# Performance work log

Measured on AMD Instinct MI355X. Metric: run time of the kernel, lower is better.

## Reference

```python
import jax, jax.numpy as jnp
import numpy as np

DIM = 1024
QK = 128
HID = 2048  # int(2 * dim)
B, N = 4, 2048
EPS = 1e-5

def setup_inputs() -> dict:
    key = jax.random.key(0)
    ks = jax.random.split(key, 8)
    std = 0.02
    return {
        "x": jax.random.normal(ks[0], (B, N, DIM), jnp.float32),
        "ln_scale": jnp.ones((DIM,), jnp.float32),
        "ln_bias": jnp.zeros((DIM,), jnp.float32),
        "W_hidden": jax.random.normal(ks[1], (DIM, 2 * HID), jnp.float32) * std,
        "b_hidden": jnp.zeros((2 * HID,), jnp.float32),
        "W_qk": jax.random.normal(ks[2], (DIM, QK), jnp.float32) * std,
        "b_qk": jnp.zeros((QK,), jnp.float32),
        "os_weight": jax.random.normal(ks[3], (2, QK), jnp.float32) * std,
        "os_bias": jnp.zeros((2, QK), jnp.float32),
        "W_out": jax.random.normal(ks[4], (HID, DIM), jnp.float32) * std,
        "b_out": jnp.zeros((DIM,), jnp.float32),
    }

def reference(x, ln_scale, ln_bias, W_hidden, b_hidden, W_qk, b_qk,
              os_weight, os_bias, W_out, b_out):
    n = x.shape[1]
    # LayerNorm over last dim
    mu = jnp.mean(x, axis=-1, keepdims=True)
    var = jnp.mean(jnp.square(x - mu), axis=-1, keepdims=True)
    xn = (x - mu) / jnp.sqrt(var + EPS) * ln_scale + ln_bias
    # to_hidden: Linear + SiLU, chunk into v, gate
    hid = jax.nn.silu(xn @ W_hidden + b_hidden)          # [B,N,2*HID]
    v, gate = hid[..., :HID], hid[..., HID:]
    # to_qk: Linear + SiLU
    qk = jax.nn.silu(xn @ W_qk + b_qk)                   # [B,N,QK]
    # offset_scale: per-head elementwise affine -> q, k
    qk2 = qk[..., None, :] * os_weight + os_bias         # [B,N,2,QK]
    q, k = qk2[..., 0, :], qk2[..., 1, :]
    # ReLU^2 attention
    sim = jnp.einsum('bid,bjd->bij', q, k) / n           # [B,N,N]
    attn = jnp.square(jax.nn.relu(sim))
    out = jnp.einsum('bij,bjd->bid', attn, v)            # [B,N,HID]
    out = out * gate
    return out @ W_out + b_out
```

## Files before the change

kernel.cpp:

```cpp
#include <hip/hip_runtime.h>
#include <math.h>

#define DIMX 1024
#define QKD  128
#define HIDD 2048
#define BATCH 4
#define SEQ  2048

typedef __bf16 bf16;
typedef __bf16 bf16x8 __attribute__((ext_vector_type(8)));
typedef __bf16 bf16x4v __attribute__((ext_vector_type(4)));
typedef float f32x4 __attribute__((ext_vector_type(4)));

__device__ __forceinline__ float siluf(float v) { return v / (1.f + expf(-v)); }
__device__ __forceinline__ void splitf(float x, bf16& h, bf16& l) {
    h = (bf16)x;
    l = (bf16)(x - (float)h);
}
__device__ __forceinline__ f32x4 mfma16(bf16x8 a, bf16x8 b, f32x4 c) {
    return __builtin_amdgcn_mfma_f32_16x16x32_bf16(a, b, c, 0, 0, 0);
}

typedef __attribute__((address_space(1))) const void cg_void;
typedef __attribute__((address_space(3))) void lds_void_t;
__device__ __forceinline__ void gload16(const bf16* g, bf16* l) {
    __builtin_amdgcn_global_load_lds((cg_void*)g, (lds_void_t*)l, 16, 0, 0);
}

template<int N> __device__ __forceinline__ void wait_vm() {
    if constexpr (N == 0)  asm volatile("s_waitcnt vmcnt(0)" ::: "memory");
    if constexpr (N == 3)  asm volatile("s_waitcnt vmcnt(3)" ::: "memory");
    if constexpr (N == 4)  asm volatile("s_waitcnt vmcnt(4)" ::: "memory");
    if constexpr (N == 6)  asm volatile("s_waitcnt vmcnt(6)" ::: "memory");
    if constexpr (N == 8)  asm volatile("s_waitcnt vmcnt(8)" ::: "memory");
}

#define SB0 __builtin_amdgcn_sched_barrier(0)

__global__ __launch_bounds__(256) void ln_split(const float* __restrict__ x,
                                                const float* __restrict__ scale,
                                                const float* __restrict__ bias,
                                                bf16* __restrict__ xh,
                                                bf16* __restrict__ xl) {
    const int row = blockIdx.x;
    const float4 v = reinterpret_cast<const float4*>(x + (size_t)row * DIMX)[threadIdx.x];
    float s  = v.x + v.y + v.z + v.w;
    float ss = v.x * v.x + v.y * v.y + v.z * v.z + v.w * v.w;
    #pragma unroll
    for (int off = 32; off; off >>= 1) {
        s  += __shfl_down(s, off);
        ss += __shfl_down(ss, off);
    }
    __shared__ float ls[4], lss[4];
    const int wid = threadIdx.x >> 6, lane = threadIdx.x & 63;
    if (lane == 0) { ls[wid] = s; lss[wid] = ss; }
    __syncthreads();
    if (threadIdx.x == 0) {
        float a = ls[0] + ls[1] + ls[2] + ls[3];
        float b = lss[0] + lss[1] + lss[2] + lss[3];
        float mu  = a / DIMX;
        float var = b / DIMX - mu * mu;
        ls[0]  = mu;
        lss[0] = rsqrtf(var + 1e-5f);
    }
    __syncthreads();
    const float mu = ls[0], rs = lss[0];
    const float4 sc = reinterpret_cast<const float4*>(scale)[threadIdx.x];
    const float4 bi = reinterpret_cast<const float4*>(bias)[threadIdx.x];
    float o[4];
    o[0] = (v.x - mu) * rs * sc.x + bi.x;
    o[1] = (v.y - mu) * rs * sc.y + bi.y;
    o[2] = (v.z - mu) * rs * sc.z + bi.z;
    o[3] = (v.w - mu) * rs * sc.w + bi.w;
    bf16x4v h, l;
    #pragma unroll
    for (int i = 0; i < 4; ++i) { bf16 hh, ll; splitf(o[i], hh, ll); h[i] = hh; l[i] = ll; }
    *reinterpret_cast<bf16x4v*>(xh + (size_t)row * DIMX + threadIdx.x * 4) = h;
    *reinterpret_cast<bf16x4v*>(xl + (size_t)row * DIMX + threadIdx.x * 4) = l;
}

__global__ __launch_bounds__(256) void wsplitT(const float* __restrict__ W, int K, int N,
                                               bf16* __restrict__ Th, bf16* __restrict__ Tl) {
    __shared__ float tile[32][33];
    const int bx = blockIdx.x * 32;
    const int by = blockIdx.y * 32;
    const int tx = threadIdx.x & 31, ty = threadIdx.x >> 5;
    #pragma unroll
    for (int r = 0; r < 32; r += 8)
        tile[ty + r][tx] = W[(size_t)(by + ty + r) * N + bx + tx];
    __syncthreads();
    #pragma unroll
    for (int r = 0; r < 32; r += 8) {
        const float v = tile[tx][ty + r];
        bf16 h, l; splitf(v, h, l);
        Th[(size_t)(bx + ty + r) * K + by + tx] = h;
        if (Tl) Tl[(size_t)(bx + ty + r) * K + by + tx] = l;
    }
}

template<int EPI, int BN>
__global__ __launch_bounds__(512) void gmm2(
    const bf16* __restrict__ A, int lda, long long sA,
    const bf16* __restrict__ B, int ldb, long long sB,
    bf16* __restrict__ O, int ldo, long long sO,
    bf16* __restrict__ G, int ldg, long long sG,
    float* __restrict__ F, int ldf,
    const float* __restrict__ e0,
    int K) {

    constexpr int BM = 256, BK = 32;
    constexpr int AE = BM * BK;
    constexpr int BE = BN * BK;
    constexpr int CHA = AE / (512 * 8);
    constexpr int CHB = BE / (512 * 8);
    constexpr int L = CHA + CHB;
    constexpr int WN = BN / 4;
    constexpr int MI = 8, NI = WN / 16;

    __shared__ __align__(16) bf16 lds[4 * (AE + BE)];

    const int z = blockIdx.z;
    A += (size_t)sA * z;
    B += (size_t)sB * z;
    bf16* Oz = O ? O + (size_t)sO * z : nullptr;
    bf16* Gz = G ? G + (size_t)sG * z : nullptr;

    const int tid = threadIdx.x;
    const int l = tid & 63, w = tid >> 6;
    const int wr = w >> 2, wc = w & 3;
    const int lr = l & 15, ls4 = l >> 4;
    const int bm = blockIdx.y * BM, bn = blockIdx.x * BN;

    const bf16* aptr[CHA];
    #pragma unroll
    for (int c = 0; c < CHA; ++c) {
        const int flat = c * 512 + tid;
        const int row = flat >> 2;
        const int slot = (flat & 3) ^ ((row >> 1) & 3);
        aptr[c] = A + (size_t)(bm + row) * lda + slot * 8;
    }
    const bf16* bptr[CHB];
    #pragma unroll
    for (int c = 0; c < CHB; ++c) {
        const int flat = c * 512 + tid;
        const int row = flat >> 2;
        const int slot = (flat & 3) ^ ((row >> 1) & 3);
        bptr[c] = B + (size_t)(bn + row) * ldb + slot * 8;
    }

    int aoff[MI], boff[NI];
    #pragma unroll
    for (int i = 0; i < MI; ++i) {
        const int row = wr * 128 + i * 16 + lr;
        aoff[i] = row * BK + (ls4 ^ ((row >> 1) & 3)) * 8;
    }
    #pragma unroll
    for (int j = 0; j < NI; ++j) {
        const int row = wc * WN + j * 16 + lr;
        boff[j] = row * BK + (ls4 ^ ((row >> 1) & 3)) * 8;
    }

    const int NT = K / BK;
    f32x4 acc[MI][NI] = {};

    auto stage = [&](int tile) {
        const int buf = tile & 3;
        bf16* ab = lds + buf * (AE + BE);
        bf16* bb = ab + AE;
        #pragma unroll
        for (int c = 0; c < CHA; ++c)
            gload16(aptr[c] + tile * BK, ab + (c * 512 + w * 64) * 8);
        #pragma unroll
        for (int c = 0; c < CHB; ++c)
            gload16(bptr[c] + tile * BK, bb + (c * 512 + w * 64) * 8);
    };

    stage(0); SB0;
    stage(1); SB0;
    stage(2); SB0;

    for (int t = 0; t < NT; ++t) {
        const int ahead = NT - 1 - t;
        if (ahead >= 2)      wait_vm<2 * L>();
        else if (ahead == 1) wait_vm<L>();
        else                 wait_vm<0>();
        __builtin_amdgcn_s_barrier();
        SB0;

        const int buf = t & 3;
        const bf16* ab = lds + buf * (AE + BE);
        const bf16* bb = ab + AE;
        bf16x8 bfr[NI], afr[MI];
        #pragma unroll
        for (int j = 0; j < NI; ++j)
            bfr[j] = *reinterpret_cast<const bf16x8*>(&bb[boff[j]]);
        #pragma unroll
        for (int i = 0; i < MI; ++i)
            afr[i] = *reinterpret_cast<const bf16x8*>(&ab[aoff[i]]);
        asm volatile("s_waitcnt lgkmcnt(0)" ::: "memory");
        SB0;
        if (t + 3 < NT) { stage(t + 3); }
        SB0;
        __builtin_amdgcn_s_setprio(1);
        #pragma unroll
        for (int i = 0; i < MI; ++i)
            #pragma unroll
            for (int j = 0; j < NI; ++j)
                acc[i][j] = mfma16(afr[i], bfr[j], acc[i][j]);
        __builtin_amdgcn_s_setprio(0);
        SB0;
    }

    #pragma unroll
    for (int i = 0; i < MI; ++i) {
        const int mf = bm + wr * 128 + i * 16 + ls4 * 4;
        #pragma unroll
        for (int j = 0; j < NI; ++j) {
            const int nn = bn + wc * WN + j * 16 + lr;
            const f32x4 a = acc[i][j];
            if constexpr (EPI == 5) {
                #pragma unroll
                for (int r = 0; r < 4; ++r) {
                    const float s = siluf(a[r] + e0[mf + r]);
                    Oz[(size_t)(mf + r) * ldo + nn] = (bf16)s;
                }
            } else if constexpr (EPI == 6) {
                #pragma unroll
                for (int r = 0; r < 4; ++r) {
                    const float s = siluf(a[r] + e0[nn]);
                    Oz[(size_t)(mf + r) * ldo + nn] = (bf16)s;
                }
            } else if constexpr (EPI == 3) {
                #pragma unroll
                for (int r = 0; r < 4; ++r) {
                    const float g = (float)Gz[(size_t)(mf + r) * ldg + nn];
                    Oz[(size_t)(mf + r) * ldo + nn] = (bf16)(a[r] * g);
                }
            } else {
                #pragma unroll
                for (int r = 0; r < 4; ++r)
                    F[(size_t)(mf + r) * ldf + nn] = a[r] + e0[nn];
            }
        }
    }
}

template<int EPI, bool SPLIT, int MI, int NI>
__global__ __launch_bounds__(256) void gmm(
    const bf16* __restrict__ Ah, const bf16* __restrict__ Al, int lda, long long sA,
    const bf16* __restrict__ Bh, const bf16* __restrict__ Bl, int ldb, long long sB,
    bf16* __restrict__ O, int ldo, long long sO,
    bf16* __restrict__ O2, bf16* __restrict__ O3, bf16* __restrict__ O4,
    const float* __restrict__ e0, const float* __restrict__ e1, const float* __restrict__ e2,
    int K, float scale) {

    constexpr int TM = MI * 32, TN = NI * 32;
    constexpr int CHA = TM / 64, CHB = TN / 64;
    __shared__ __align__(16) bf16 As[TM * 32];
    __shared__ __align__(16) bf16 Bs[TN * 32];

    const int z = blockIdx.z;
    Ah += (size_t)sA * z;
    if (SPLIT) Al += (size_t)sA * z;
    Bh += (size_t)sB * z;
    if (SPLIT) Bl += (size_t)sB * z;
    if (O) O += (size_t)sO * z;

    const int t = threadIdx.x;
    const int l = t & 63, w = t >> 6;
    const int wr = w >> 1, wc = w & 1;
    const int lr = l & 15, ls = l >> 4;
    const int bm = blockIdx.y * TM, bn = blockIdx.x * TN;

    f32x4 acc[MI][NI] = {};
    const int KT = SPLIT ? 3 * K : K;

    for (int k0 = 0; k0 < KT; k0 += 32) {
        const bf16 *pA, *pB;
        int kin;
        if constexpr (SPLIT) {
            if (k0 < K)          { pA = Ah; pB = Bh; kin = k0; }
            else if (k0 < 2 * K) { pA = Al; pB = Bh; kin = k0 - K; }
            else                 { pA = Ah; pB = Bl; kin = k0 - 2 * K; }
        } else { pA = Ah; pB = Bh; kin = k0; }

        #pragma unroll
        for (int c = 0; c < CHA; ++c) {
            const int idx = c * 256 + w * 64 + l;
            const int row = idx >> 2;
            const int sg = (idx & 3) ^ ((row >> 1) & 3);
            gload16(pA + (size_t)(bm + row) * lda + kin + sg * 8,
                    As + (size_t)(c * 256 + w * 64) * 8);
        }
        #pragma unroll
        for (int c = 0; c < CHB; ++c) {
            const int idx = c * 256 + w * 64 + l;
            const int row = idx >> 2;
            const int sg = (idx & 3) ^ ((row >> 1) & 3);
            gload16(pB + (size_t)(bn + row) * ldb + kin + sg * 8,
                    Bs + (size_t)(c * 256 + w * 64) * 8);
        }
        __syncthreads();

        bf16x8 bfr[NI];
        #pragma unroll
        for (int j = 0; j < NI; ++j) {
            const int row = wc * (NI * 16) + j * 16 + lr;
            const int sl = ls ^ ((row >> 1) & 3);
            bfr[j] = *reinterpret_cast<const bf16x8*>(&Bs[row * 32 + sl * 8]);
        }
        #pragma unroll
        for (int i = 0; i < MI; ++i) {
            const int row = wr * (MI * 16) + i * 16 + lr;
            const int sl = ls ^ ((row >> 1) & 3);
            const bf16x8 af = *reinterpret_cast<const bf16x8*>(&As[row * 32 + sl * 8]);
            #pragma unroll
            for (int j = 0; j < NI; ++j)
                acc[i][j] = mfma16(af, bfr[j], acc[i][j]);
        }
        __syncthreads();
    }

    #pragma unroll
    for (int i = 0; i < MI; ++i) {
        const int mf = bm + wr * (MI * 16) + i * 16 + ls * 4;
        #pragma unroll
        for (int j = 0; j < NI; ++j) {
            const int nn = bn + wc * (NI * 16) + j * 16 + lr;
            const f32x4 a = acc[i][j];
            if constexpr (EPI == 1) {
                #pragma unroll
                for (int r = 0; r < 4; ++r) {
                    const float s = siluf(a[r] + e0[nn]);
                    const float q = s * e1[nn] + e2[nn];
                    const float k = s * e1[QKD + nn] + e2[QKD + nn];
                    bf16 h, lo;
                    splitf(q, h, lo);
                    O[(size_t)(mf + r) * ldo + nn] = h;  O2[(size_t)(mf + r) * ldo + nn] = lo;
                    splitf(k, h, lo);
                    O3[(size_t)(mf + r) * ldo + nn] = h; O4[(size_t)(mf + r) * ldo + nn] = lo;
                }
            } else if constexpr (EPI == 2) {
                #pragma unroll
                for (int r = 0; r < 4; ++r) {
                    const float tv = a[r] * scale;
                    const float p = tv > 0.f ? tv * tv : 0.f;
                    O[(size_t)(mf + r) * ldo + nn] = (bf16)p;
                }
            }
        }
    }
}

extern "C" void kernel_launch(void* const* d_in, const int* in_sizes, int n_in,
                              void* d_out, int out_size, void* d_ws, size_t ws_size,
                              hipStream_t stream) {
    const float* x        = (const float*)d_in[0];
    const float* ln_scale = (const float*)d_in[1];
    const float* ln_bias  = (const float*)d_in[2];
    const float* W_hidden = (const float*)d_in[3];
    const float* b_hidden = (const float*)d_in[4];
    const float* W_qk     = (const float*)d_in[5];
    const float* b_qk     = (const float*)d_in[6];
    const float* os_w     = (const float*)d_in[7];
    const float* os_b     = (const float*)d_in[8];
    const float* W_out    = (const float*)d_in[9];
    const float* b_out    = (const float*)d_in[10];
    float* out = (float*)d_out;

    char* p = (char*)d_ws;
    bf16* WhTh  = (bf16*)p; p += (size_t)4096 * 1024 * 2;
    bf16* WqkTh = (bf16*)p; p += (size_t)128 * 1024 * 2;
    bf16* WqkTl = (bf16*)p; p += (size_t)128 * 1024 * 2;
    bf16* WoTh  = (bf16*)p; p += (size_t)1024 * 2048 * 2;

    wsplitT<<<dim3(4096 / 32, 1024 / 32), 256, 0, stream>>>(W_hidden, 1024, 4096, WhTh, nullptr);
    wsplitT<<<dim3(128 / 32, 1024 / 32), 256, 0, stream>>>(W_qk, 1024, 128, WqkTh, WqkTl);
    wsplitT<<<dim3(1024 / 32, 2048 / 32), 256, 0, stream>>>(W_out, 2048, 1024, WoTh, nullptr);

    const size_t used = (size_t)(p - (char*)d_ws);
    const size_t qkB   = (size_t)4 * 8192 * 128 * 2;
    const size_t vTB   = (size_t)2048 * 8192 * 2;
    const size_t gateB = (size_t)8192 * 2048 * 2;
    const size_t attnB = (size_t)4 * 2048 * 2048 * 2;
    const size_t yB    = (size_t)8192 * 2048 * 2;
    const bool allb = (ws_size >= used + qkB + vTB + gateB + attnB + yB + (1u << 20));

    if (allb) {
        bf16* xh = (bf16*)out;
        bf16* xl = xh + (size_t)8192 * 1024;
        bf16* qh   = (bf16*)p; p += (size_t)8192 * 128 * 2;
        bf16* ql   = (bf16*)p; p += (size_t)8192 * 128 * 2;
        bf16* kh   = (bf16*)p; p += (size_t)8192 * 128 * 2;
        bf16* kl   = (bf16*)p; p += (size_t)8192 * 128 * 2;
        bf16* vT   = (bf16*)p; p += vTB;
        bf16* gate = (bf16*)p; p += gateB;
        bf16* attn = (bf16*)p; p += attnB;
        bf16* y    = (bf16*)p; p += yB;

        ln_split<<<8192, 256, 0, stream>>>(x, ln_scale, ln_bias, xh, xl);

        gmm2<5, 256><<<dim3(8192 / 256, 2048 / 256), 512, 0, stream>>>(
            WhTh, 1024, 0, xh, 1024, 0,
            vT, 8192, 0, nullptr, 0, 0,
            nullptr, 0, b_hidden, 1024);

        gmm2<6, 256><<<dim3(2048 / 256, 8192 / 256), 512, 0, stream>>>(
            xh, 1024, 0, WhTh + (size_t)2048 * 1024, 1024, 0,
            gate, 2048, 0, nullptr, 0, 0,
            nullptr, 0, b_hidden + HIDD, 1024);

        gmm<1, true, 2, 2><<<dim3(128 / 64, 8192 / 64), 256, 0, stream>>>(
            xh, xl, 1024, 0, WqkTh, WqkTl, 1024, 0,
            qh, 128, 0, ql, kh, kl,
            b_qk, os_w, os_b, 1024, 0.f);

        gmm<2, true, 4, 4><<<dim3(16, 16, 4), 256, 0, stream>>>(
            qh, ql, 128, (long long)2048 * 128, kh, kl, 128, (long long)2048 * 128,
            attn, 2048, (long long)2048 * 2048, nullptr, nullptr, nullptr,
            nullptr, nullptr, nullptr, 128, 1.0f / SEQ);

        gmm2<3, 256><<<dim3(2048 / 256, 2048 / 256, 4), 512, 0, stream>>>(
            attn, 2048, (long long)2048 * 2048, vT, 8192, 2048,
            y, 2048, (long long)2048 * 2048, gate, 2048, (long long)2048 * 2048,
            nullptr, 0, nullptr, 2048);

        gmm2<4, 128><<<dim3(1024 / 128, 8192 / 256), 512, 0, stream>>>(
            y, 2048, 0, WoTh, 2048, 0,
            nullptr, 0, 0, nullptr, 0, 0,
            out, 1024, b_out, 2048);
    } else {
        bf16* xh = (bf16*)p; p += (size_t)8192 * 1024 * 2;
        bf16* xl = (bf16*)p; p += (size_t)8192 * 1024 * 2;
        bf16* qh   = (bf16*)p; p += (size_t)2048 * 128 * 2;
        bf16* ql   = (bf16*)p; p += (size_t)2048 * 128 * 2;
        bf16* kh   = (bf16*)p; p += (size_t)2048 * 128 * 2;
        bf16* kl   = (bf16*)p; p += (size_t)2048 * 128 * 2;
        bf16* vT   = (bf16*)p; p += (size_t)2048 * 2048 * 2;
        bf16* gate = (bf16*)p; p += (size_t)2048 * 2048 * 2;
        bf16* attn = (bf16*)p; p += (size_t)2048 * 2048 * 2;
        bf16* y    = (bf16*)p; p += (size_t)2048 * 2048 * 2;

        ln_split<<<8192, 256, 0, stream>>>(x, ln_scale, ln_bias, xh, xl);

        for (int b = 0; b < BATCH; ++b) {
            const bf16* xhb = xh + (size_t)b * 2048 * 1024;
            const bf16* xlb = xl + (size_t)b * 2048 * 1024;

            gmm2<5, 256><<<dim3(2048 / 256, 2048 / 256), 512, 0, stream>>>(
                WhTh, 1024, 0, xhb, 1024, 0,
                vT, 2048, 0, nullptr, 0, 0,
                nullptr, 0, b_hidden, 1024);

            gmm2<6, 256><<<dim3(2048 / 256, 2048 / 256), 512, 0, stream>>>(
                xhb, 1024, 0, WhTh + (size_t)2048 * 1024, 1024, 0,
                gate, 2048, 0, nullptr, 0, 0,
                nullptr, 0, b_hidden + HIDD, 1024);

            gmm<1, true, 2, 2><<<dim3(128 / 64, 2048 / 64), 256, 0, stream>>>(
                xhb, xlb, 1024, 0, WqkTh, WqkTl, 1024, 0,
                qh, 128, 0, ql, kh, kl,
                b_qk, os_w, os_b, 1024, 0.f);

            gmm<2, true, 4, 4><<<dim3(16, 16, 1), 256, 0, stream>>>(
                qh, ql, 128, 0, kh, kl, 128, 0,
                attn, 2048, 0, nullptr, nullptr, nullptr,
                nullptr, nullptr, nullptr, 128, 1.0f / SEQ);

            gmm2<3, 256><<<dim3(2048 / 256, 2048 / 256, 1), 512, 0, stream>>>(
                attn, 2048, 0, vT, 2048, 0,
                y, 2048, 0, gate, 2048, 0,
                nullptr, 0, nullptr, 2048);

            gmm2<4, 128><<<dim3(1024 / 128, 2048 / 256), 512, 0, stream>>>(
                y, 2048, 0, WoTh, 2048, 0,
                nullptr, 0, 0, nullptr, 0, 0,
                out + (size_t)b * 2048 * 1024, 1024, b_out, 2048);
        }
    }
}
```

Baseline: 293.5 us.

## Concatenate split-bf16 Q/K into K=384 operands and reuse big-tile GEMM for QK^T

The q and k hi/lo parts are now stored as concatenated rows [qh|ql|qh] and [kh|kh|kl], so the three-term split-precision product qh*kh + ql*kh + qh*kl becomes a single plain bf16 GEMM with K=384. That GEMM then runs on the larger 256x256-tile gmm2 kernel with a new ReLU² epilogue, replacing the split-aware gmm kernel. The QK projection kernel's tile is also enlarged. The aim is better MFMA utilization and fewer kernel variants. The cost is 3x wider Q/K buffers and a dropped lo*lo term, which the old split kernel probably also skipped.

```diff
diff --git a/kernel.cpp b/kernel.cpp
--- a/kernel.cpp
+++ b/kernel.cpp
@@ -106,7 +106,7 @@
     bf16* __restrict__ G, int ldg, long long sG,
     float* __restrict__ F, int ldf,
     const float* __restrict__ e0,
-    int K) {
+    int K, float scale) {
 
     constexpr int BM = 256, BK = 32;
     constexpr int AE = BM * BK;
@@ -230,6 +230,13 @@
                     const float s = siluf(a[r] + e0[nn]);
                     Oz[(size_t)(mf + r) * ldo + nn] = (bf16)s;
                 }
+            } else if constexpr (EPI == 2) {
+                #pragma unroll
+                for (int r = 0; r < 4; ++r) {
+                    const float tv = a[r] * scale;
+                    const float pv = tv > 0.f ? tv * tv : 0.f;
+                    Oz[(size_t)(mf + r) * ldo + nn] = (bf16)pv;
+                }
             } else if constexpr (EPI == 3) {
                 #pragma unroll
                 for (int r = 0; r < 4; ++r) {
@@ -334,18 +341,12 @@
                     const float s = siluf(a[r] + e0[nn]);
                     const float q = s * e1[nn] + e2[nn];
                     const float k = s * e1[QKD + nn] + e2[QKD + nn];
-                    bf16 h, lo;
-                    splitf(q, h, lo);
-                    O[(size_t)(mf + r) * ldo + nn] = h;  O2[(size_t)(mf + r) * ldo + nn] = lo;
-                    splitf(k, h, lo);
-                    O3[(size_t)(mf + r) * ldo + nn] = h; O4[(size_t)(mf + r) * ldo + nn] = lo;
-                }
-            } else if constexpr (EPI == 2) {
-                #pragma unroll
-                for (int r = 0; r < 4; ++r) {
-                    const float tv = a[r] * scale;
-                    const float p = tv > 0.f ? tv * tv : 0.f;
-                    O[(size_t)(mf + r) * ldo + nn] = (bf16)p;
+                    bf16 qh_, ql_, kh_, kl_;
+                    splitf(q, qh_, ql_);
+                    splitf(k, kh_, kl_);
+                    const size_t base = (size_t)(mf + r) * ldo;
+                    O[base + nn] = qh_;  O[base + QKD + nn] = ql_;  O[base + 2 * QKD + nn] = qh_;
+                    O3[base + nn] = kh_; O3[base + QKD + nn] = kh_; O3[base + 2 * QKD + nn] = kl_;
                 }
             }
         }
@@ -379,20 +380,19 @@
     wsplitT<<<dim3(1024 / 32, 2048 / 32), 256, 0, stream>>>(W_out, 2048, 1024, WoTh, nullptr);
 
     const size_t used = (size_t)(p - (char*)d_ws);
-    const size_t qkB   = (size_t)4 * 8192 * 128 * 2;
+    const size_t qcB   = (size_t)8192 * 384 * 2;
+    const size_t kcB   = (size_t)8192 * 384 * 2;
     const size_t vTB   = (size_t)2048 * 8192 * 2;
     const size_t gateB = (size_t)8192 * 2048 * 2;
     const size_t attnB = (size_t)4 * 2048 * 2048 * 2;
     const size_t yB    = (size_t)8192 * 2048 * 2;
-    const bool allb = (ws_size >= used + qkB + vTB + gateB + attnB + yB + (1u << 20));
+    const bool allb = (ws_size >= used + qcB + kcB + vTB + gateB + attnB + yB + (1u << 20));
 
     if (allb) {
         bf16* xh = (bf16*)out;
         bf16* xl = xh + (size_t)8192 * 1024;
-        bf16* qh   = (bf16*)p; p += (size_t)8192 * 128 * 2;
-        bf16* ql   = (bf16*)p; p += (size_t)8192 * 128 * 2;
-        bf16* kh   = (bf16*)p; p += (size_t)8192 * 128 * 2;
-        bf16* kl   = (bf16*)p; p += (size_t)8192 * 128 * 2;
+        bf16* qcat = (bf16*)p; p += qcB;
+        bf16* kcat = (bf16*)p; p += kcB;
         bf16* vT   = (bf16*)p; p += vTB;
         bf16* gate = (bf16*)p; p += gateB;
         bf16* attn = (bf16*)p; p += attnB;
@@ -403,39 +403,37 @@
         gmm2<5, 256><<<dim3(8192 / 256, 2048 / 256), 512, 0, stream>>>(
             WhTh, 1024, 0, xh, 1024, 0,
             vT, 8192, 0, nullptr, 0, 0,
-            nullptr, 0, b_hidden, 1024);
+            nullptr, 0, b_hidden, 1024, 0.f);
 
         gmm2<6, 256><<<dim3(2048 / 256, 8192 / 256), 512, 0, stream>>>(
             xh, 1024, 0, WhTh + (size_t)2048 * 1024, 1024, 0,
             gate, 2048, 0, nullptr, 0, 0,
-            nullptr, 0, b_hidden + HIDD, 1024);
-
-        gmm<1, true, 2, 2><<<dim3(128 / 64, 8192 / 64), 256, 0, stream>>>(
+            nullptr, 0, b_hidden + HIDD, 1024, 0.f);
+
+        gmm<1, true, 4, 2><<<dim3(128 / 64, 8192 / 128), 256, 0, stream>>>(
             xh, xl, 1024, 0, WqkTh, WqkTl, 1024, 0,
-            qh, 128, 0, ql, kh, kl,
+            qcat, 384, 0, nullptr, kcat, nullptr,
             b_qk, os_w, os_b, 1024, 0.f);
 
-        gmm<2, true, 4, 4><<<dim3(16, 16, 4), 256, 0, stream>>>(
-            qh, ql, 128, (long long)2048 * 128, kh, kl, 128, (long long)2048 * 128,
-            attn, 2048, (long long)2048 * 2048, nullptr, nullptr, nullptr,
-            nullptr, nullptr, nullptr, 128, 1.0f / SEQ);
+        gmm2<2, 256><<<dim3(2048 / 256, 2048 / 256, 4), 512, 0, stream>>>(
+            qcat, 384, (long long)2048 * 384, kcat, 384, (long long)2048 * 384,
+            attn, 2048, (long long)2048 * 2048, nullptr, 0, 0,
+            nullptr, 0, nullptr, 384, 1.0f / SEQ);
 
         gmm2<3, 256><<<dim3(2048 / 256, 2048 / 256, 4), 512, 0, stream>>>(
             attn, 2048, (long long)2048 * 2048, vT, 8192, 2048,
             y, 2048, (long long)2048 * 2048, gate, 2048, (long long)2048 * 2048,
-            nullptr, 0, nullptr, 2048);
+            nullptr, 0, nullptr, 2048, 0.f);
 
         gmm2<4, 128><<<dim3(1024 / 128, 8192 / 256), 512, 0, stream>>>(
             y, 2048, 0, WoTh, 2048, 0,
             nullptr, 0, 0, nullptr, 0, 0,
-            out, 1024, b_out, 2048);
+            out, 1024, b_out, 2048, 0.f);
     } else {
         bf16* xh = (bf16*)p; p += (size_t)8192 * 1024 * 2;
         bf16* xl = (bf16*)p; p += (size_t)8192 * 1024 * 2;
-        bf16* qh   = (bf16*)p; p += (size_t)2048 * 128 * 2;
-        bf16* ql   = (bf16*)p; p += (size_t)2048 * 128 * 2;
-        bf16* kh   = (bf16*)p; p += (size_t)2048 * 128 * 2;
-        bf16* kl   = (bf16*)p; p += (size_t)2048 * 128 * 2;
+        bf16* qcat = (bf16*)p; p += (size_t)2048 * 384 * 2;
+        bf16* kcat = (bf16*)p; p += (size_t)2048 * 384 * 2;
         bf16* vT   = (bf16*)p; p += (size_t)2048 * 2048 * 2;
         bf16* gate = (bf16*)p; p += (size_t)2048 * 2048 * 2;
         bf16* attn = (bf16*)p; p += (size_t)2048 * 2048 * 2;
@@ -450,32 +448,32 @@
             gmm2<5, 256><<<dim3(2048 / 256, 2048 / 256), 512, 0, stream>>>(
                 WhTh, 1024, 0, xhb, 1024, 0,
                 vT, 2048, 0, nullptr, 0, 0,
-                nullptr, 0, b_hidden, 1024);
+                nullptr, 0, b_hidden, 1024, 0.f);
 
             gmm2<6, 256><<<dim3(2048 / 256, 2048 / 256), 512, 0, stream>>>(
                 xhb, 1024, 0, WhTh + (size_t)2048 * 1024, 1024, 0,
                 gate, 2048, 0, nullptr, 0, 0,
-                nullptr, 0, b_hidden + HIDD, 1024);
-
-            gmm<1, true, 2, 2><<<dim3(128 / 64, 2048 / 64), 256, 0, stream>>>(
+                nullptr, 0, b_hidden + HIDD, 1024, 0.f);
+
+            gmm<1, true, 4, 2><<<dim3(128 / 64, 2048 / 128), 256, 0, stream>>>(
                 xhb, xlb, 1024, 0, WqkTh, WqkTl, 1024, 0,
-                qh, 128, 0, ql, kh, kl,
+                qcat, 384, 0, nullptr, kcat, nullptr,
                 b_qk, os_w, os_b, 1024, 0.f);
 
-            gmm<2, true, 4, 4><<<dim3(16, 16, 1), 256, 0, stream>>>(
-                qh, ql, 128, 0, kh, kl, 128, 0,
-                attn, 2048, 0, nullptr, nullptr, nullptr,
-                nullptr, nullptr, nullptr, 128, 1.0f / SEQ);
+            gmm2<2, 256><<<dim3(2048 / 256, 2048 / 256, 1), 512, 0, stream>>>(
+                qcat, 384, 0, kcat, 384, 0,
+                attn, 2048, 0, nullptr, 0, 0,
+                nullptr, 0, nullptr, 384, 1.0f / SEQ);
 
             gmm2<3, 256><<<dim3(2048 / 256, 2048 / 256, 1), 512, 0, stream>>>(
                 attn, 2048, 0, vT, 2048, 0,
                 y, 2048, 0, gate, 2048, 0,
-                nullptr, 0, nullptr, 2048);
+                nullptr, 0, nullptr, 2048, 0.f);
 
             gmm2<4, 128><<<dim3(1024 / 128, 2048 / 256), 512, 0, stream>>>(
                 y, 2048, 0, WoTh, 2048, 0,
                 nullptr, 0, 0, nullptr, 0, 0,
-                out + (size_t)b * 2048 * 1024, 1024, b_out, 2048);
-        }
-    }
-}
+                out + (size_t)b * 2048 * 1024, 1024, b_out, 2048, 0.f);
+        }
+    }
+}
```

Measured after the change: 302.8 us. 3.2% more time.

## Split-K the output projection into two fp32 partials with separate bias-add pass

Applied to the files above, without the earlier changes.

Replaces the final output GEMM with a split-K version that runs two K halves as separate grid slices, writing fp32 partial results into workspace. A new elementwise kernel then sums the partials and adds the output bias. The aim is to double the block count so more compute units stay busy. The cost is extra fp32 write and read traffic plus one more kernel launch.

```diff
diff --git a/kernel.cpp b/kernel.cpp
--- a/kernel.cpp
+++ b/kernel.cpp
@@ -95,6 +95,24 @@
         bf16 h, l; splitf(v, h, l);
         Th[(size_t)(bx + ty + r) * K + by + tx] = h;
         if (Tl) Tl[(size_t)(bx + ty + r) * K + by + tx] = l;
+    }
+}
+
+__global__ __launch_bounds__(256) void addbias(const float* __restrict__ p0,
+                                               const float* __restrict__ p1,
+                                               const float* __restrict__ b,
+                                               float* __restrict__ out,
+                                               int total4) {
+    for (int i = blockIdx.x * 256 + threadIdx.x; i < total4; i += gridDim.x * 256) {
+        const float4 a = reinterpret_cast<const float4*>(p0)[i];
+        const float4 c = reinterpret_cast<const float4*>(p1)[i];
+        const int col = (i & (DIMX / 4 - 1)) * 4;
+        float4 r;
+        r.x = a.x + c.x + b[col + 0];
+        r.y = a.y + c.y + b[col + 1];
+        r.z = a.z + c.z + b[col + 2];
+        r.w = a.w + c.w + b[col + 3];
+        reinterpret_cast<float4*>(out)[i] = r;
     }
 }
 
@@ -245,6 +263,117 @@
     }
 }
 
+__global__ __launch_bounds__(512) void gmm8(
+    const bf16* __restrict__ A, int lda, long long sA,
+    const bf16* __restrict__ B, int ldb, long long sB,
+    float* __restrict__ F, int ldf, long long sF,
+    int K) {
+
+    constexpr int BM = 256, BN = 128, BK = 32;
+    constexpr int AE = BM * BK;
+    constexpr int BE = BN * BK;
+    constexpr int TE = AE + BE;
+    constexpr int CHA = 2, CHB = 1, L = 3;
+    constexpr int MI = 8, NI = 2;
+
+    __shared__ __align__(16) bf16 lds[3 * TE];
+
+    const int z = blockIdx.z;
+    A += (size_t)sA * z;
+    B += (size_t)sB * z;
+    float* Fz = F + (size_t)sF * z;
+
+    const int tid = threadIdx.x;
+    const int l = tid & 63, w = tid >> 6;
+    const int wr = w >> 2, wc = w & 3;
+    const int lr = l & 15, ls4 = l >> 4;
+    const int bm = blockIdx.y * BM, bn = blockIdx.x * BN;
+
+    const bf16* aptr[CHA];
+    #pragma unroll
+    for (int c = 0; c < CHA; ++c) {
+        const int flat = c * 512 + tid;
+        const int row = flat >> 2;
+        const int slot = (flat & 3) ^ ((row >> 1) & 3);
+        aptr[c] = A + (size_t)(bm + row) * lda + slot * 8;
+    }
+    const bf16* bptr;
+    {
+        const int row = tid >> 2;
+        const int slot = (tid & 3) ^ ((row >> 1) & 3);
+        bptr = B + (size_t)(bn + row) * ldb + slot * 8;
+    }
+
+    int aoff[MI], boff[NI];
+    #pragma unroll
+    for (int i = 0; i < MI; ++i) {
+        const int row = wr * 128 + i * 16 + lr;
+        aoff[i] = row * BK + (ls4 ^ ((row >> 1) & 3)) * 8;
+    }
+    #pragma unroll
+    for (int j = 0; j < NI; ++j) {
+        const int row = wc * 32 + j * 16 + lr;
+        boff[j] = row * BK + (ls4 ^ ((row >> 1) & 3)) * 8;
+    }
+
+    const int NT = K / BK;
+    f32x4 acc[MI][NI] = {};
+
+    auto stage = [&](int tile) {
+        bf16* ab = lds + (tile % 3) * TE;
+        bf16* bb = ab + AE;
+        #pragma unroll
+        for (int c = 0; c < CHA; ++c)
+            gload16(aptr[c] + (size_t)tile * BK, ab + (c * 512 + w * 64) * 8);
+        gload16(bptr + (size_t)tile * BK, bb + w * 64 * 8);
+    };
+
+    stage(0); SB0;
+    stage(1); SB0;
+
+    for (int t = 0; t < NT; ++t) {
+        if (t + 1 < NT) wait_vm<L>();
+        else            wait_vm<0>();
+        __builtin_amdgcn_s_barrier();
+        SB0;
+
+        const bf16* ab = lds + (t % 3) * TE;
+        const bf16* bb = ab + AE;
+        bf16x8 afr[MI], bfr[NI];
+        #pragma unroll
+        for (int j = 0; j < NI; ++j)
+            bfr[j] = *reinterpret_cast<const bf16x8*>(&bb[boff[j]]);
+        #pragma unroll
+        for (int i = 0; i < MI; ++i)
+            afr[i] = *reinterpret_cast<const bf16x8*>(&ab[aoff[i]]);
+        asm volatile("s_waitcnt lgkmcnt(0)" ::: "memory");
+        SB0;
+        if (t + 2 < NT) { stage(t + 2); }
+        SB0;
+        __builtin_amdgcn_s_setprio(1);
+        #pragma unroll
+        for (int i = 0; i < MI; ++i)
+            #pragma unroll
+            for (int j = 0; j < NI; ++j)
+                acc[i][j] = mfma16(afr[i], bfr[j], acc[i][j]);
+        __builtin_amdgcn_s_setprio(0);
+        SB0;
+    }
+
+    #pragma unroll
+    for (int i = 0; i < MI; ++i) {
+        const int mf = bm + wr * 128 + i * 16 + ls4 * 4;
+        #pragma unroll
+        for (int j = 0; j < NI; ++j) {
+            const int nn = bn + wc * 32 + j * 16 + lr;
+            const f32x4 a = acc[i][j];
+            #pragma unroll
+            for (int r = 0; r < 4; ++r)
+                Fz[(size_t)(mf + r) * ldf + nn] = a[r];
+        }
+    }
+}
+
 template<int EPI, bool SPLIT, int MI, int NI>
 __global__ __launch_bounds__(256) void gmm(
     const bf16* __restrict__ Ah, const bf16* __restrict__ Al, int lda, long long sA,
@@ -398,6 +527,9 @@
         bf16* attn = (bf16*)p; p += attnB;
         bf16* y    = (bf16*)p; p += yB;
 
+        float* outp0 = (float*)qh;
+        float* outp1 = outp0 + (size_t)8192 * 1024;
+
         ln_split<<<8192, 256, 0, stream>>>(x, ln_scale, ln_bias, xh, xl);
 
         gmm2<5, 256><<<dim3(8192 / 256, 2048 / 256), 512, 0, stream>>>(
@@ -425,10 +557,11 @@
             y, 2048, (long long)2048 * 2048, gate, 2048, (long long)2048 * 2048,
             nullptr, 0, nullptr, 2048);
 
-        gmm2<4, 128><<<dim3(1024 / 128, 8192 / 256), 512, 0, stream>>>(
-            y, 2048, 0, WoTh, 2048, 0,
-            nullptr, 0, 0, nullptr, 0, 0,
-            out, 1024, b_out, 2048);
+        gmm8<<<dim3(1024 / 128, 8192 / 256, 2), 512, 0, stream>>>(
+            y, 2048, 1024, WoTh, 2048, 1024,
+            outp0, 1024, (long long)8192 * 1024, 1024);
+
+        addbias<<<2048, 256, 0, stream>>>(outp0, outp1, b_out, out, 8192 * 1024 / 4);
     } else {
         bf16* xh = (bf16*)p; p += (size_t)8192 * 1024 * 2;
         bf16* xl = (bf16*)p; p += (size_t)8192 * 1024 * 2;
```

Result: slower. 318.8 us (+8.6%).
